# Kernel tuning notes

Hardware: AMD Instinct MI355X
Metric: run time of the kernel (lower is better)

The kernel has to match this reference:

```python
import jax, jax.numpy as jnp
import numpy as np

NQ = 4  # qubits; statevector is (2,2,2,2)
H_GATE = jnp.array([[1.0, 1.0], [1.0, -1.0]], dtype=jnp.complex64) / jnp.sqrt(jnp.float32(2.0))


def _rot(p):
    # PennyLane Rot(phi, theta, omega) = RZ(omega) RY(theta) RZ(phi)
    phi, theta, omega = p[0], p[1], p[2]
    c = jnp.cos(theta * 0.5).astype(jnp.complex64)
    s = jnp.sin(theta * 0.5).astype(jnp.complex64)
    ep = jnp.exp(-0.5j * (phi + omega).astype(jnp.complex64))  # e^{-i(phi+omega)/2}
    em = jnp.exp(-0.5j * (phi - omega).astype(jnp.complex64))  # e^{-i(phi-omega)/2}
    m00 = ep * c
    m01 = -jnp.conj(em) * s
    m10 = em * s
    m11 = jnp.conj(ep) * c
    return jnp.stack([jnp.stack([m00, m01]), jnp.stack([m10, m11])])


def _crot(p):
    # Controlled-Rot: block diag(I2, Rot)
    U = _rot(p)
    I2 = jnp.eye(2, dtype=U.dtype)
    Z = jnp.zeros((2, 2), dtype=U.dtype)
    return jnp.concatenate([jnp.concatenate([I2, Z], axis=1), jnp.concatenate([Z, U], axis=1)], axis=0)


def _apply1(state, U, w):
    s = jnp.tensordot(U, state, axes=((1,), (w,)))
    return jnp.moveaxis(s, 0, w)


def _apply2(state, U4, c, t):
    G = U4.reshape(2, 2, 2, 2)
    s = jnp.tensordot(G, state, axes=((2, 3), (c, t)))
    return jnp.moveaxis(s, (0, 1), (c, t))


def _block(state, params):
    # params: [4, NQ, 3]. Layer 0: per-qubit Rot; layers 1..3: CRot with offsets 1,2,3.
    for q in range(NQ):
        state = _apply1(state, _rot(params[0, q]), q)
    for bi, off in enumerate((1, 2, 3), start=1):
        for q in range(NQ):
            tgt = (q + off) % NQ
            state = _apply2(state, _crot(params[bi, q]), q, tgt)
    return state


def _init_state():
    # |0000> then Hadamard on every wire
    s = jnp.zeros((2,) * NQ, dtype=jnp.complex64).at[(0,) * NQ].set(1.0)
    for q in range(NQ):
        s = _apply1(s, H_GATE, q)
    return s


def _score(s_par, p_par, e_par):
    s0 = _init_state()
    sp = _block(_block(s0, s_par), p_par)  # sp_circuit state
    eo = _block(s0, e_par)                 # e_circuit state
    # Re(vdot(eo, sp)) = Re(sum conj(eo) * sp)
    return jnp.real(jnp.sum(jnp.conj(eo) * sp))


def setup_inputs():
    key = jax.random.key(0)
    k1, k2, k3, k4, k5 = jax.random.split(key, 5)
    E, R, B = 100000, 1000, 131072
    lim = np.pi / 10
    return {
        "entity_params": jax.random.uniform(k1, (E, 4, NQ, 3), jnp.float32, -lim, lim),
        "relation_params": jax.random.uniform(k2, (R, 4, NQ, 3), jnp.float32, -lim, lim),
        "h": jax.random.randint(k3, (B,), 0, E),
        "r": jax.random.randint(k4, (B,), 0, R),
        "t": jax.random.randint(k5, (B,), 0, E),
    }


def reference(entity_params, relation_params, h, r, t):
    s_par = entity_params[h]      # [B, 4, NQ, 3]
    p_par = relation_params[r]
    e_par = entity_params[t]
    return jax.vmap(_score)(s_par, p_par, e_par)  # [B]
```

## Files before the change

kernel.cpp:

```cpp
#include <hip/hip_runtime.h>


struct c32 { float x, y; };

__device__ __forceinline__ c32 cmul(c32 a, c32 b) {
    return { a.x * b.x - a.y * b.y, a.x * b.y + a.y * b.x };
}
__device__ __forceinline__ c32 cadd(c32 a, c32 b) { return { a.x + b.x, a.y + b.y }; }

__device__ __forceinline__ void make_rot(float phi, float th, float om,
                                         c32& m00, c32& m01, c32& m10, c32& m11) {
    float st, ct;
    __sincosf(0.5f * th, &st, &ct);
    float sp_, cp_;
    __sincosf(-0.5f * (phi + om), &sp_, &cp_);
    float sm_, cm_;
    __sincosf(-0.5f * (phi - om), &sm_, &cm_);
    m00 = {  cp_ * ct,  sp_ * ct };
    m01 = { -cm_ * st,  sm_ * st };
    m10 = {  cm_ * st,  sm_ * st };
    m11 = {  cp_ * ct, -sp_ * ct };
}

__device__ __forceinline__ void load48(float* dst, const float* __restrict__ src) {
    const float4* s4 = reinterpret_cast<const float4*>(src);
    float4* d4 = reinterpret_cast<float4*>(dst);
#pragma unroll
    for (int i = 0; i < 12; ++i) d4[i] = s4[i];
}

__device__ __forceinline__ void apply_block(c32* s, const float* p) {
#pragma unroll
    for (int q = 0; q < 4; ++q) {
        c32 m00, m01, m10, m11;
        make_rot(p[q * 3 + 0], p[q * 3 + 1], p[q * 3 + 2], m00, m01, m10, m11);
        const int tmask = 1 << (3 - q);
#pragma unroll
        for (int i = 0; i < 16; ++i) {
            if ((i & tmask) == 0) {
                c32 a = s[i], b = s[i | tmask];
                s[i]         = cadd(cmul(m00, a), cmul(m01, b));
                s[i | tmask] = cadd(cmul(m10, a), cmul(m11, b));
            }
        }
    }
#pragma unroll
    for (int off = 1; off <= 3; ++off) {
#pragma unroll
        for (int q = 0; q < 4; ++q) {
            const int pi = (off * 4 + q) * 3;
            c32 m00, m01, m10, m11;
            make_rot(p[pi + 0], p[pi + 1], p[pi + 2], m00, m01, m10, m11);
            const int tq = (q + off) & 3;
            const int cmask = 1 << (3 - q);
            const int tmask = 1 << (3 - tq);
#pragma unroll
            for (int i = 0; i < 16; ++i) {
                if ((i & cmask) != 0 && (i & tmask) == 0) {
                    c32 a = s[i], b = s[i | tmask];
                    s[i]         = cadd(cmul(m00, a), cmul(m01, b));
                    s[i | tmask] = cadd(cmul(m10, a), cmul(m11, b));
                }
            }
        }
    }
}

__global__ __launch_bounds__(256) void qkge_kernel(
    const float* __restrict__ ent, const float* __restrict__ rel,
    const int* __restrict__ h, const int* __restrict__ r, const int* __restrict__ t,
    float* __restrict__ out, int B) {
    const int b = blockIdx.x * blockDim.x + threadIdx.x;
    if (b >= B) return;

    float pbuf[48];

    c32 sp[16];
#pragma unroll
    for (int i = 0; i < 16; ++i) sp[i] = { 0.25f, 0.0f };
    load48(pbuf, ent + (long long)h[b] * 48);
    apply_block(sp, pbuf);
    load48(pbuf, rel + (long long)r[b] * 48);
    apply_block(sp, pbuf);

    c32 eo[16];
#pragma unroll
    for (int i = 0; i < 16; ++i) eo[i] = { 0.25f, 0.0f };
    load48(pbuf, ent + (long long)t[b] * 48);
    apply_block(eo, pbuf);

    float acc = 0.0f;
#pragma unroll
    for (int i = 0; i < 16; ++i) acc += eo[i].x * sp[i].x + eo[i].y * sp[i].y;
    out[b] = acc;
}

extern "C" void kernel_launch(void* const* d_in, const int* in_sizes, int n_in,
                              void* d_out, int out_size, void* d_ws, size_t ws_size,
                              hipStream_t stream) {
    const float* ent = (const float*)d_in[0];
    const float* rel = (const float*)d_in[1];
    const int*   h   = (const int*)d_in[2];
    const int*   r   = (const int*)d_in[3];
    const int*   t   = (const int*)d_in[4];
    float* out = (float*)d_out;
    const int B = in_sizes[2];

    const int block = 256;
    const int grid = (B + block - 1) / block;
    qkge_kernel<<<grid, block, 0, stream>>>(ent, rel, h, r, t, out, B);
}
```

Measured before the change: 101.5 us.

## Precompute per-entity states and per-relation gate matrices before batch scoring

Splits the single kernel into three. One kernel simulates each entity's block once into a 16-amplitude state, one builds the 16 rotation matrices for each relation, and a final batch kernel gathers the h state, applies the relation gates and takes a dot product with the t state. Each of the 100k entities is simulated once instead of once per batch occurrence, and the batch kernel no longer does sincos work. In exchange it runs three launches, writes and reads state buffers in workspace, and simulates all entities even when the batch references only some of them.

```diff
diff --git a/kernel.cpp b/kernel.cpp
--- a/kernel.cpp
+++ b/kernel.cpp
@@ -20,13 +20,6 @@
     m01 = { -cm_ * st,  sm_ * st };
     m10 = {  cm_ * st,  sm_ * st };
     m11 = {  cp_ * ct, -sp_ * ct };
-}
-
-__device__ __forceinline__ void load48(float* dst, const float* __restrict__ src) {
-    const float4* s4 = reinterpret_cast<const float4*>(src);
-    float4* d4 = reinterpret_cast<float4*>(dst);
-#pragma unroll
-    for (int i = 0; i < 12; ++i) d4[i] = s4[i];
 }
 
 __device__ __forceinline__ void apply_block(c32* s, const float* p) {
@@ -66,32 +59,102 @@
     }
 }
 
-__global__ __launch_bounds__(256) void qkge_kernel(
-    const float* __restrict__ ent, const float* __restrict__ rel,
+__global__ __launch_bounds__(256) void k1_entity_states(
+    const float* __restrict__ ent, float* __restrict__ estate, int E) {
+    const int e = blockIdx.x * blockDim.x + threadIdx.x;
+    if (e >= E) return;
+    float pbuf[48];
+    const float4* s4 = reinterpret_cast<const float4*>(ent + (long long)e * 48);
+    float4* d4 = reinterpret_cast<float4*>(pbuf);
+#pragma unroll
+    for (int i = 0; i < 12; ++i) d4[i] = s4[i];
+
+    c32 s[16];
+#pragma unroll
+    for (int i = 0; i < 16; ++i) s[i] = { 0.25f, 0.0f };
+    apply_block(s, pbuf);
+
+    float4* o4 = reinterpret_cast<float4*>(estate + (long long)e * 32);
+#pragma unroll
+    for (int i = 0; i < 8; ++i) {
+        o4[i] = make_float4(s[2 * i].x, s[2 * i].y, s[2 * i + 1].x, s[2 * i + 1].y);
+    }
+}
+
+__global__ __launch_bounds__(256) void k2_relation_mats(
+    const float* __restrict__ rel, float* __restrict__ relmat, int R) {
+    const int idx = blockIdx.x * blockDim.x + threadIdx.x;
+    if (idx >= R * 16) return;
+    const int rr = idx >> 4, g = idx & 15;
+    const float* p = rel + (long long)rr * 48 + g * 3;
+    c32 m00, m01, m10, m11;
+    make_rot(p[0], p[1], p[2], m00, m01, m10, m11);
+    float4* o4 = reinterpret_cast<float4*>(relmat + (long long)idx * 8);
+    o4[0] = make_float4(m00.x, m00.y, m01.x, m01.y);
+    o4[1] = make_float4(m10.x, m10.y, m11.x, m11.y);
+}
+
+__global__ __launch_bounds__(256) void k3_batch(
+    const float* __restrict__ estate, const float* __restrict__ relmat,
     const int* __restrict__ h, const int* __restrict__ r, const int* __restrict__ t,
     float* __restrict__ out, int B) {
     const int b = blockIdx.x * blockDim.x + threadIdx.x;
     if (b >= B) return;
 
-    float pbuf[48];
+    c32 sp[16];
+    {
+        const float4* s4 = reinterpret_cast<const float4*>(estate + (long long)h[b] * 32);
+#pragma unroll
+        for (int i = 0; i < 8; ++i) {
+            float4 v = s4[i];
+            sp[2 * i]     = { v.x, v.y };
+            sp[2 * i + 1] = { v.z, v.w };
+        }
+    }
 
-    c32 sp[16];
+    const float4* rm4 = reinterpret_cast<const float4*>(relmat + (long long)r[b] * 128);
 #pragma unroll
-    for (int i = 0; i < 16; ++i) sp[i] = { 0.25f, 0.0f };
-    load48(pbuf, ent + (long long)h[b] * 48);
-    apply_block(sp, pbuf);
-    load48(pbuf, rel + (long long)r[b] * 48);
-    apply_block(sp, pbuf);
-
-    c32 eo[16];
+    for (int g = 0; g < 16; ++g) {
+        float4 a4 = rm4[2 * g], b4 = rm4[2 * g + 1];
+        c32 m00 = { a4.x, a4.y }, m01 = { a4.z, a4.w };
+        c32 m10 = { b4.x, b4.y }, m11 = { b4.z, b4.w };
+        if (g < 4) {
+            const int tmask = 1 << (3 - g);
 #pragma unroll
-    for (int i = 0; i < 16; ++i) eo[i] = { 0.25f, 0.0f };
-    load48(pbuf, ent + (long long)t[b] * 48);
-    apply_block(eo, pbuf);
+            for (int i = 0; i < 16; ++i) {
+                if ((i & tmask) == 0) {
+                    c32 a = sp[i], bb = sp[i | tmask];
+                    sp[i]         = cadd(cmul(m00, a), cmul(m01, bb));
+                    sp[i | tmask] = cadd(cmul(m10, a), cmul(m11, bb));
+                }
+            }
+        } else {
+            const int off = 1 + ((g - 4) >> 2);
+            const int q = (g - 4) & 3;
+            const int tq = (q + off) & 3;
+            const int cmask = 1 << (3 - q);
+            const int tmask = 1 << (3 - tq);
+#pragma unroll
+            for (int i = 0; i < 16; ++i) {
+                if ((i & cmask) != 0 && (i & tmask) == 0) {
+                    c32 a = sp[i], bb = sp[i | tmask];
+                    sp[i]         = cadd(cmul(m00, a), cmul(m01, bb));
+                    sp[i | tmask] = cadd(cmul(m10, a), cmul(m11, bb));
+                }
+            }
+        }
+    }
 
     float acc = 0.0f;
+    {
+        const float4* s4 = reinterpret_cast<const float4*>(estate + (long long)t[b] * 32);
 #pragma unroll
-    for (int i = 0; i < 16; ++i) acc += eo[i].x * sp[i].x + eo[i].y * sp[i].y;
+        for (int i = 0; i < 8; ++i) {
+            float4 v = s4[i];
+            acc += v.x * sp[2 * i].x + v.y * sp[2 * i].y;
+            acc += v.z * sp[2 * i + 1].x + v.w * sp[2 * i + 1].y;
+        }
+    }
     out[b] = acc;
 }
 
@@ -104,9 +167,15 @@
     const int*   r   = (const int*)d_in[3];
     const int*   t   = (const int*)d_in[4];
     float* out = (float*)d_out;
+
+    const int E = in_sizes[0] / 48;
+    const int R = in_sizes[1] / 48;
     const int B = in_sizes[2];
 
-    const int block = 256;
-    const int grid = (B + block - 1) / block;
-    qkge_kernel<<<grid, block, 0, stream>>>(ent, rel, h, r, t, out, B);
+    float* estate = (float*)d_ws;
+    float* relmat = estate + (size_t)E * 32;
+
+    k2_relation_mats<<<(R * 16 + 255) / 256, 256, 0, stream>>>(rel, relmat, R);
+    k1_entity_states<<<(E + 255) / 256, 256, 0, stream>>>(ent, estate, E);
+    k3_batch<<<(B + 255) / 256, 256, 0, stream>>>(estate, relmat, h, r, t, out, B);
 }
```

New measurement: 99.78 us. About the same (-1.7%).

## Precompute per-entity circuit states and gate matrices, then score the batch

Applied to the files above, without the earlier changes.

The work is split into several kernels. The first builds every gate matrix once for all entities and relations. The next computes the post-block statevector once per entity (100k of them) instead of twice per batch element. The final batch kernel then only gathers the h and t states and applies the relation block. This removes redundant trig and entity-block work, but adds extra launches and a large materialised matrix buffer (E×128 floats) that is written and then read back, along with random gathers of 128-byte states.

```diff
diff --git a/kernel.cpp b/kernel.cpp
--- a/kernel.cpp
+++ b/kernel.cpp
@@ -22,72 +22,92 @@
     m11 = {  cp_ * ct, -sp_ * ct };
 }
 
-__device__ __forceinline__ void load48(float* dst, const float* __restrict__ src) {
-    const float4* s4 = reinterpret_cast<const float4*>(src);
-    float4* d4 = reinterpret_cast<float4*>(dst);
-#pragma unroll
-    for (int i = 0; i < 12; ++i) d4[i] = s4[i];
+__global__ __launch_bounds__(256) void k_build_mats(
+    const float* __restrict__ par, float* __restrict__ mats, int N) {
+    const int idx = blockIdx.x * blockDim.x + threadIdx.x;
+    if (idx >= N * 16) return;
+    const int n = idx >> 4, g = idx & 15;
+    const float* p = par + (long long)n * 48 + g * 3;
+    c32 m00, m01, m10, m11;
+    make_rot(p[0], p[1], p[2], m00, m01, m10, m11);
+    float4* o4 = reinterpret_cast<float4*>(mats + (long long)idx * 8);
+    o4[0] = make_float4(m00.x, m00.y, m01.x, m01.y);
+    o4[1] = make_float4(m10.x, m10.y, m11.x, m11.y);
 }
 
-__device__ __forceinline__ void apply_block(c32* s, const float* p) {
+__device__ __forceinline__ void apply_block_mats(c32* s, const float4* __restrict__ m4) {
 #pragma unroll
-    for (int q = 0; q < 4; ++q) {
-        c32 m00, m01, m10, m11;
-        make_rot(p[q * 3 + 0], p[q * 3 + 1], p[q * 3 + 2], m00, m01, m10, m11);
-        const int tmask = 1 << (3 - q);
+    for (int g = 0; g < 16; ++g) {
+        float4 a4 = m4[2 * g], b4 = m4[2 * g + 1];
+        c32 m00 = { a4.x, a4.y }, m01 = { a4.z, a4.w };
+        c32 m10 = { b4.x, b4.y }, m11 = { b4.z, b4.w };
+        if (g < 4) {
+            const int tmask = 1 << (3 - g);
 #pragma unroll
-        for (int i = 0; i < 16; ++i) {
-            if ((i & tmask) == 0) {
-                c32 a = s[i], b = s[i | tmask];
-                s[i]         = cadd(cmul(m00, a), cmul(m01, b));
-                s[i | tmask] = cadd(cmul(m10, a), cmul(m11, b));
+            for (int i = 0; i < 16; ++i) {
+                if ((i & tmask) == 0) {
+                    c32 a = s[i], bb = s[i | tmask];
+                    s[i]         = cadd(cmul(m00, a), cmul(m01, bb));
+                    s[i | tmask] = cadd(cmul(m10, a), cmul(m11, bb));
+                }
             }
-        }
-    }
-#pragma unroll
-    for (int off = 1; off <= 3; ++off) {
-#pragma unroll
-        for (int q = 0; q < 4; ++q) {
-            const int pi = (off * 4 + q) * 3;
-            c32 m00, m01, m10, m11;
-            make_rot(p[pi + 0], p[pi + 1], p[pi + 2], m00, m01, m10, m11);
+        } else {
+            const int off = 1 + ((g - 4) >> 2);
+            const int q = (g - 4) & 3;
             const int tq = (q + off) & 3;
             const int cmask = 1 << (3 - q);
             const int tmask = 1 << (3 - tq);
 #pragma unroll
             for (int i = 0; i < 16; ++i) {
                 if ((i & cmask) != 0 && (i & tmask) == 0) {
-                    c32 a = s[i], b = s[i | tmask];
-                    s[i]         = cadd(cmul(m00, a), cmul(m01, b));
-                    s[i | tmask] = cadd(cmul(m10, a), cmul(m11, b));
+                    c32 a = s[i], bb = s[i | tmask];
+                    s[i]         = cadd(cmul(m00, a), cmul(m01, bb));
+                    s[i | tmask] = cadd(cmul(m10, a), cmul(m11, bb));
                 }
             }
         }
     }
 }
 
-__global__ __launch_bounds__(256) void qkge_kernel(
-    const float* __restrict__ ent, const float* __restrict__ rel,
+__global__ __launch_bounds__(256) void k1b_entity_states(
+    const float* __restrict__ emat, float* __restrict__ estate, int E) {
+    const int e = blockIdx.x * blockDim.x + threadIdx.x;
+    if (e >= E) return;
+    c32 s[16];
+#pragma unroll
+    for (int i = 0; i < 16; ++i) s[i] = { 0.25f, 0.0f };
+    const float4* m4 = reinterpret_cast<const float4*>(emat + (long long)e * 128);
+    apply_block_mats(s, m4);
+    float4* o4 = reinterpret_cast<float4*>(estate + (long long)e * 32);
+#pragma unroll
+    for (int i = 0; i < 8; ++i)
+        o4[i] = make_float4(s[2 * i].x, s[2 * i].y, s[2 * i + 1].x, s[2 * i + 1].y);
+}
+
+__global__ __launch_bounds__(256) void k3_batch(
+    const float* __restrict__ estate, const float* __restrict__ relmat,
     const int* __restrict__ h, const int* __restrict__ r, const int* __restrict__ t,
     float* __restrict__ out, int B) {
     const int b = blockIdx.x * blockDim.x + threadIdx.x;
     if (b >= B) return;
 
-    float pbuf[48];
+    const int hb = h[b], rb = r[b], tb = t[b];
 
-    c32 sp[16];
+    const float4* h4 = reinterpret_cast<const float4*>(estate + (long long)hb * 32);
+    const float4* t4 = reinterpret_cast<const float4*>(estate + (long long)tb * 32);
+    c32 sp[16], eo[16];
 #pragma unroll
-    for (int i = 0; i < 16; ++i) sp[i] = { 0.25f, 0.0f };
-    load48(pbuf, ent + (long long)h[b] * 48);
-    apply_block(sp, pbuf);
-    load48(pbuf, rel + (long long)r[b] * 48);
-    apply_block(sp, pbuf);
+    for (int i = 0; i < 8; ++i) {
+        float4 hv = h4[i];
+        float4 tv = t4[i];
+        sp[2 * i]     = { hv.x, hv.y };
+        sp[2 * i + 1] = { hv.z, hv.w };
+        eo[2 * i]     = { tv.x, tv.y };
+        eo[2 * i + 1] = { tv.z, tv.w };
+    }
 
-    c32 eo[16];
-#pragma unroll
-    for (int i = 0; i < 16; ++i) eo[i] = { 0.25f, 0.0f };
-    load48(pbuf, ent + (long long)t[b] * 48);
-    apply_block(eo, pbuf);
+    const float4* rm4 = reinterpret_cast<const float4*>(relmat + (long long)rb * 128);
+    apply_block_mats(sp, rm4);
 
     float acc = 0.0f;
 #pragma unroll
@@ -104,9 +124,17 @@
     const int*   r   = (const int*)d_in[3];
     const int*   t   = (const int*)d_in[4];
     float* out = (float*)d_out;
+
+    const int E = in_sizes[0] / 48;
+    const int R = in_sizes[1] / 48;
     const int B = in_sizes[2];
 
-    const int block = 256;
-    const int grid = (B + block - 1) / block;
-    qkge_kernel<<<grid, block, 0, stream>>>(ent, rel, h, r, t, out, B);
+    float* emat   = (float*)d_ws;
+    float* relmat = emat + (size_t)E * 128;
+    float* estate = relmat + (size_t)R * 128;
+
+    k_build_mats<<<(E * 16 + 255) / 256, 256, 0, stream>>>(ent, emat, E);
+    k_build_mats<<<(R * 16 + 255) / 256, 256, 0, stream>>>(rel, relmat, R);
+    k1b_entity_states<<<(E + 255) / 256, 256, 0, stream>>>(emat, estate, E);
+    k3_batch<<<(B + 255) / 256, 256, 0, stream>>>(estate, relmat, h, r, t, out, B);
 }
```

After: 118.9 us. 1.17x slower.
